# Performance work log

Hardware: AMD Instinct MI355X
Metric: run time of the kernel (lower is better)

Reference implementation:

```python
import jax, jax.numpy as jnp
from jax import lax
import numpy as np

# dims: batch, in_channels, out_channels, spatial, kernel, padding
B, IC, OC, H, W, K, PAD = 4, 64, 64, 32, 32, 3, 1


def setup_inputs() -> dict:
    key = jax.random.key(0)
    k1, k2, k3, k4 = jax.random.split(key, 4)
    # x is a binary (+/-1) activation in this stochastic binary network
    x = jnp.sign(jax.random.normal(k1, (B, IC, H, W), jnp.float32))
    x = jnp.where(x == 0, 1.0, x)
    # q: small per-unit correction probabilities
    q = jax.random.uniform(k2, (B, IC, H, W), jnp.float32) * 1e-3
    # xavier_uniform with sigmoid gain (=1.0), as in _reset_parameters
    fan_in, fan_out = IC * K * K, OC * K * K
    bound = float(np.sqrt(6.0 / (fan_in + fan_out)))
    weight = jax.random.uniform(k3, (OC, IC, K, K), jnp.float32, -bound, bound)
    bbound = float(1.0 / np.sqrt(fan_in))
    bias = jax.random.uniform(k4, (OC,), jnp.float32, -bbound, bbound)
    return {"x": x, "q": q, "weight": weight, "bias": bias}


def _forward(x, q, weight, bias, key):
    pad = 2 * (K // 2) - PAD  # = 1 for k=3, padding=1
    # a0 = conv(x), NCHW / OIHW
    a0 = lax.conv_general_dilated(x, weight, (1, 1), [(PAD, PAD), (PAD, PAD)]) \
         + bias[None, :, None, None]                      # [B,OC,H,W]
    p0 = jax.nn.sigmoid(a0)
    # stochastic binary sample new_x in {-1,+1}; sample is non-differentiable
    new_x = 2.0 * jax.random.bernoulli(key, p0).astype(p0.dtype) - 1.0

    Kf = jnp.flip(weight, (2, 3))                         # flipped kernel
    a0_ = jnp.pad(a0, ((0, 0), (0, 0), (pad, pad), (pad, pad)))     # [B,OC,H+K-1,W+K-1]
    p0_ = jnp.pad(p0, ((0, 0), (0, 0), (pad, pad), (pad, pad)))
    y_ = jnp.pad(new_x, ((0, 0), (0, 0), (pad, pad), (pad, pad)))

    # Fused version of _compute_conv_diffs + _compute_delta_sum: instead of
    # materializing the full [K,K,B,OC,IC,H,W] tensor, process each (l1,l2)
    # shift (K*K = 9 static iterations), same math.
    delta_q = jnp.zeros((B, OC, H + K - 1, W + K - 1), p0.dtype)
    for l1 in range(K):
        for l2 in range(K):
            # a[l1,l2] : pre-activation if input bit (l1,l2) were flipped
            a_l = a0_[:, :, None, l1:l1 + H, l2:l2 + W] \
                  - 2.0 * x[:, None] * Kf[None, :, :, l1, l2, None, None]  # [B,OC,IC,H,W]
            p_l = jax.nn.sigmoid(a_l)
            add = jnp.sum((p_l - p0_[:, :, None, l1:l1 + H, l2:l2 + W]) * q[:, None],
                          axis=2) * (-y_[:, :, l1:l1 + H, l2:l2 + W])       # [B,OC,H,W]
            delta_q = delta_q.at[:, :, l1:l1 + H, l2:l2 + W].add(add)
    delta_q = delta_q[:, :, pad:-pad, pad:-pad]           # [B,OC,H,W]

    # delta_0: zero in value, carries gradient of p0 (straight-through trick)
    delta_0 = -new_x * (p0 - lax.stop_gradient(p0))
    qs = jnp.sum(q, axis=(1, 2, 3), keepdims=True)        # [B,1,1,1]
    new_q = delta_0 * (1.0 - qs) + delta_q
    # stride == 1 -> the [::stride] slicing is a no-op
    return new_x, new_q


def reference(x, q, weight, bias):
    return _forward(x, q, weight, bias, jax.random.key(42))
```

## Files before the change

### kernel.cpp

```cpp
#include <hip/hip_runtime.h>
#include <cstdint>


typedef __attribute__((ext_vector_type(4))) int   i32x4;
typedef __attribute__((ext_vector_type(8))) short s16x8;
typedef __attribute__((ext_vector_type(4))) float f32x4;

static constexpr int OFF_X8   = 0;
static constexpr int OFF_XQH  = 295936;
static constexpr int OFF_WD   = 887808;
static constexpr int OFF_WB   = 1035264;

__device__ __forceinline__ uint32_t rotl32(uint32_t v, int n) {
  return (v << n) | (v >> (32 - n));
}

__device__ __forceinline__ unsigned short f2bf(float f) {
  uint32_t u = __float_as_uint(f);
  uint32_t r = (u + 0x7FFFu + ((u >> 16) & 1u)) >> 16;
  return (unsigned short)r;
}

__device__ __forceinline__ float threefry_u(uint32_t j) {
  uint32_t x0 = 0u, x1 = j;
  const uint32_t ks1 = 42u, ks2 = 0x1BD11BDAu ^ 42u;
  x0 += 0u; x1 += ks1;
#define QR(rot) { x0 += x1; x1 = rotl32(x1, rot); x1 ^= x0; }
  QR(13) QR(15) QR(26) QR(6)
  x0 += ks1; x1 += ks2 + 1u;
  QR(17) QR(29) QR(16) QR(24)
  x0 += ks2; x1 += 0u + 2u;
  QR(13) QR(15) QR(26) QR(6)
  x0 += 0u; x1 += ks1 + 3u;
  QR(17) QR(29) QR(16) QR(24)
  x0 += ks1; x1 += ks2 + 4u;
  QR(13) QR(15) QR(26) QR(6)
  x0 += ks2; x1 += 0u + 5u;
#undef QR
  uint32_t bits = x0 ^ x1;
  return __uint_as_float((bits >> 9) | 0x3F800000u) - 1.0f;
}

__global__ __launch_bounds__(256) void prep_kernel(
    const float* __restrict__ x, const float* __restrict__ q,
    const float* __restrict__ weight, char* __restrict__ ws) {
  const int blk = blockIdx.x;
  const int tid = threadIdx.x;

  if (blk < 128) {
    const int b = blk >> 5;
    const int h = blk & 31;
    __shared__ char           x8s[2048];
    __shared__ unsigned short xqs[2048];
    const int ic = tid >> 2;
    const int w0 = (tid & 3) * 8;
    const int src = ((b * 64 + ic) * 32 + h) * 32 + w0;
    float4 xa = *(const float4*)(x + src);
    float4 xb = *(const float4*)(x + src + 4);
    float4 qa = *(const float4*)(q + src);
    float4 qb = *(const float4*)(q + src + 4);
    float xv[8] = {xa.x, xa.y, xa.z, xa.w, xb.x, xb.y, xb.z, xb.w};
    float qv[8] = {qa.x, qa.y, qa.z, qa.w, qb.x, qb.y, qb.z, qb.w};
#pragma unroll
    for (int j = 0; j < 8; ++j) {
      int a = (w0 + j) * 64 + ic;
      x8s[a] = (char)(int)xv[j];
      xqs[a] = f2bf(xv[j] * qv[j]);
    }
    __syncthreads();
    const int rowel = ((b * 34 + h + 1) * 34 + 1) * 64;
    ((uint2*)(ws + OFF_X8 + rowel))[tid]      = ((const uint2*)x8s)[tid];
    ((uint4*)(ws + OFF_XQH + rowel * 2))[tid] = ((const uint4*)xqs)[tid];
  } else if (blk < 132) {
    const int b = blk - 128;
    for (int k = tid; k < 8448; k += 256) {
      int cell = k >> 6;
      int ic = k & 63;
      int hp, wp;
      if (cell < 34)       { hp = 0;          wp = cell; }
      else if (cell < 68)  { hp = 33;         wp = cell - 34; }
      else if (cell < 100) { hp = cell - 67;  wp = 0; }
      else                 { hp = cell - 99;  wp = 33; }
      int a = ((b * 34 + hp) * 34 + wp) * 64 + ic;
      ((char*)(ws + OFF_X8))[a] = 0;
      ((unsigned short*)(ws + OFF_XQH))[a] = 0;
    }
  } else {
    int k  = (blk - 132) * 256 + tid;
    int ic = k & 63;
    int t  = k >> 6;
    int oc  = t & 63;
    int tap = t >> 6;
    int kh = tap / 3, kw = tap % 3;
    float Wv = weight[((oc * 64 + ic) * 3 + kh) * 3 + kw];
    long long wi = llrint((double)Wv * 2147483648.0);
    char* wd = ws + OFF_WD;
#pragma unroll
    for (int dig = 0; dig < 4; ++dig) {
      signed char d = (signed char)(wi & 0xFF);
      wd[dig * 36864 + k] = d;
      wi = (wi - (long long)d) >> 8;
    }
    ((unsigned short*)(ws + OFF_WB))[k]  = f2bf(Wv);
  }
}

__global__ __launch_bounds__(256, 1) void main_kernel(
    const char* __restrict__ ws, const float* __restrict__ bias,
    float* __restrict__ out) {
  const char* x8            = ws + OFF_X8;
  const unsigned short* xqh = (const unsigned short*)(ws + OFF_XQH);
  const char* wd            = ws + OFF_WD;
  const unsigned short* wb  = (const unsigned short*)(ws + OFF_WB);

  const int b  = blockIdx.x >> 6;
  const int h  = (blockIdx.x >> 1) & 31;
  const int nt = blockIdx.x & 1;

  const int octile = threadIdx.x >> 6;
  const int lane   = threadIdx.x & 63;
  const int quad   = lane >> 4;
  const int l16    = lane & 15;

  i32x4 bI[9];
  s16x8 bX[9][2];
#pragma unroll
  for (int kh = 0; kh < 3; ++kh) {
#pragma unroll
    for (int kw = 0; kw < 3; ++kw) {
      const int t = kh * 3 + kw;
      const int pix = ((b * 34 + h + kh) * 34 + (nt * 16 + l16 + kw)) * 64;
      bI[t]    = *(const i32x4*)(x8 + pix + quad * 16);
      bX[t][0] = *(const s16x8*)(xqh + pix + quad * 8);
      bX[t][1] = *(const s16x8*)(xqh + pix + 32 + quad * 8);
    }
  }

  i32x4 accI[4];
#pragma unroll
  for (int d = 0; d < 4; ++d) accI[d] = (i32x4){0, 0, 0, 0};
  f32x4 aC1 = {0.f, 0.f, 0.f, 0.f};

  const int aoff_i8 = (octile * 16 + l16) * 64 + quad * 16;
  const int aoff_bf = (octile * 16 + l16) * 64 + quad * 8;

#pragma unroll
  for (int tap = 0; tap < 9; ++tap) {
    i32x4 aI[4];
#pragma unroll
    for (int d = 0; d < 4; ++d)
      aI[d] = *(const i32x4*)(wd + d * 36864 + tap * 4096 + aoff_i8);
    s16x8 aW0 = *(const s16x8*)(wb + tap * 4096 + aoff_bf);
    s16x8 aW1 = *(const s16x8*)(wb + tap * 4096 + aoff_bf + 32);
#pragma unroll
    for (int d = 0; d < 4; ++d)
      accI[d] = __builtin_amdgcn_mfma_i32_16x16x64_i8(aI[d], bI[tap], accI[d], 0, 0, 0);
    aC1 = __builtin_amdgcn_mfma_f32_16x16x32_bf16(aW0, bX[tap][0], aC1, 0, 0, 0);
    aC1 = __builtin_amdgcn_mfma_f32_16x16x32_bf16(aW1, bX[tap][1], aC1, 0, 0, 0);
  }

  const int w = nt * 16 + l16;
#pragma unroll
  for (int r = 0; r < 4; ++r) {
    const int ocr = octile * 16 + quad * 4 + r;
    double a0 = (((double)accI[3][r] * 256.0 + (double)accI[2][r]) * 256.0 +
                 (double)accI[1][r]) * 256.0 + (double)accI[0][r];
    a0 = a0 * (1.0 / 2147483648.0) + (double)bias[ocr];
    double p0d = 1.0 / (1.0 + exp(-a0));
    const int o = ((b * 64 + ocr) * 32 + h) * 32 + w;
    float su = threefry_u((uint32_t)o);
    float nx = ((double)su < p0d) ? 1.0f : -1.0f;
    float p0 = (float)p0d;
    float s1 = p0 * (1.0f - p0);
    float dq = 2.0f * nx * s1 * aC1[r];
    out[o] = nx;
    out[262144 + o] = dq;
  }
}

extern "C" void kernel_launch(void* const* d_in, const int* in_sizes, int n_in,
                              void* d_out, int out_size, void* d_ws, size_t ws_size,
                              hipStream_t stream) {
  const float* x      = (const float*)d_in[0];
  const float* q      = (const float*)d_in[1];
  const float* weight = (const float*)d_in[2];
  const float* bias   = (const float*)d_in[3];
  float* out = (float*)d_out;
  char* ws   = (char*)d_ws;

  prep_kernel<<<276, 256, 0, stream>>>(x, q, weight, ws);
  main_kernel<<<256, 256, 0, stream>>>(ws, bias, out);
}
```

Measured before the change: 71.16 us.

## Fuse activation repacking into main kernel via padded shared-memory tiles

```diff
diff --git a/kernel.cpp b/kernel.cpp
--- a/kernel.cpp
+++ b/kernel.cpp
@@ -6,10 +6,11 @@
 typedef __attribute__((ext_vector_type(8))) short s16x8;
 typedef __attribute__((ext_vector_type(4))) float f32x4;
 
-static constexpr int OFF_X8   = 0;
-static constexpr int OFF_XQH  = 295936;
-static constexpr int OFF_WD   = 887808;
-static constexpr int OFF_WB   = 1035264;
+static constexpr int OFF_WD = 0;
+static constexpr int OFF_WB = 147456;
+
+static constexpr int X8_STRIDE = 80;
+static constexpr int XQ_STRIDE = 72;
 
 __device__ __forceinline__ uint32_t rotl32(uint32_t v, int n) {
   return (v << n) | (v >> (32 - n));
@@ -41,87 +42,82 @@
   return __uint_as_float((bits >> 9) | 0x3F800000u) - 1.0f;
 }
 
-__global__ __launch_bounds__(256) void prep_kernel(
-    const float* __restrict__ x, const float* __restrict__ q,
+__global__ __launch_bounds__(256) void wprep_kernel(
     const float* __restrict__ weight, char* __restrict__ ws) {
-  const int blk = blockIdx.x;
-  const int tid = threadIdx.x;
-
-  if (blk < 128) {
-    const int b = blk >> 5;
-    const int h = blk & 31;
-    __shared__ char           x8s[2048];
-    __shared__ unsigned short xqs[2048];
-    const int ic = tid >> 2;
-    const int w0 = (tid & 3) * 8;
-    const int src = ((b * 64 + ic) * 32 + h) * 32 + w0;
-    float4 xa = *(const float4*)(x + src);
-    float4 xb = *(const float4*)(x + src + 4);
-    float4 qa = *(const float4*)(q + src);
-    float4 qb = *(const float4*)(q + src + 4);
-    float xv[8] = {xa.x, xa.y, xa.z, xa.w, xb.x, xb.y, xb.z, xb.w};
-    float qv[8] = {qa.x, qa.y, qa.z, qa.w, qb.x, qb.y, qb.z, qb.w};
+  int k  = blockIdx.x * 256 + threadIdx.x;
+  int ic = k & 63;
+  int t  = k >> 6;
+  int oc  = t & 63;
+  int tap = t >> 6;
+  int kh = tap / 3, kw = tap % 3;
+  float Wv = weight[((oc * 64 + ic) * 3 + kh) * 3 + kw];
+  long long wi = llrint((double)Wv * 2147483648.0);
+  char* wd = ws + OFF_WD;
 #pragma unroll
-    for (int j = 0; j < 8; ++j) {
-      int a = (w0 + j) * 64 + ic;
-      x8s[a] = (char)(int)xv[j];
-      xqs[a] = f2bf(xv[j] * qv[j]);
-    }
-    __syncthreads();
-    const int rowel = ((b * 34 + h + 1) * 34 + 1) * 64;
-    ((uint2*)(ws + OFF_X8 + rowel))[tid]      = ((const uint2*)x8s)[tid];
-    ((uint4*)(ws + OFF_XQH + rowel * 2))[tid] = ((const uint4*)xqs)[tid];
-  } else if (blk < 132) {
-    const int b = blk - 128;
-    for (int k = tid; k < 8448; k += 256) {
-      int cell = k >> 6;
-      int ic = k & 63;
-      int hp, wp;
-      if (cell < 34)       { hp = 0;          wp = cell; }
-      else if (cell < 68)  { hp = 33;         wp = cell - 34; }
-      else if (cell < 100) { hp = cell - 67;  wp = 0; }
-      else                 { hp = cell - 99;  wp = 33; }
-      int a = ((b * 34 + hp) * 34 + wp) * 64 + ic;
-      ((char*)(ws + OFF_X8))[a] = 0;
-      ((unsigned short*)(ws + OFF_XQH))[a] = 0;
-    }
-  } else {
-    int k  = (blk - 132) * 256 + tid;
-    int ic = k & 63;
-    int t  = k >> 6;
-    int oc  = t & 63;
-    int tap = t >> 6;
-    int kh = tap / 3, kw = tap % 3;
-    float Wv = weight[((oc * 64 + ic) * 3 + kh) * 3 + kw];
-    long long wi = llrint((double)Wv * 2147483648.0);
-    char* wd = ws + OFF_WD;
-#pragma unroll
-    for (int dig = 0; dig < 4; ++dig) {
-      signed char d = (signed char)(wi & 0xFF);
-      wd[dig * 36864 + k] = d;
-      wi = (wi - (long long)d) >> 8;
-    }
-    ((unsigned short*)(ws + OFF_WB))[k]  = f2bf(Wv);
+  for (int dig = 0; dig < 4; ++dig) {
+    signed char d = (signed char)(wi & 0xFF);
+    wd[dig * 36864 + k] = d;
+    wi = (wi - (long long)d) >> 8;
   }
+  ((unsigned short*)(ws + OFF_WB))[k] = f2bf(Wv);
 }
 
 __global__ __launch_bounds__(256, 1) void main_kernel(
+    const float* __restrict__ x, const float* __restrict__ q,
     const char* __restrict__ ws, const float* __restrict__ bias,
     float* __restrict__ out) {
-  const char* x8            = ws + OFF_X8;
-  const unsigned short* xqh = (const unsigned short*)(ws + OFF_XQH);
-  const char* wd            = ws + OFF_WD;
-  const unsigned short* wb  = (const unsigned short*)(ws + OFF_WB);
+  const char* wd           = ws + OFF_WD;
+  const unsigned short* wb = (const unsigned short*)(ws + OFF_WB);
+
+  __shared__ __align__(16) char           x8s[3 * 34 * X8_STRIDE];
+  __shared__ __align__(16) unsigned short xqs[3 * 34 * XQ_STRIDE];
 
   const int b  = blockIdx.x >> 6;
   const int h  = (blockIdx.x >> 1) & 31;
   const int nt = blockIdx.x & 1;
+  const int tid = threadIdx.x;
 
-  const int octile = threadIdx.x >> 6;
-  const int lane   = threadIdx.x & 63;
+  {
+    int* z1 = (int*)x8s;
+#pragma unroll
+    for (int i = tid; i < 3 * 34 * X8_STRIDE / 4; i += 256) z1[i] = 0;
+    int* z2 = (int*)xqs;
+#pragma unroll
+    for (int i = tid; i < 3 * 34 * XQ_STRIDE / 2; i += 256) z2[i] = 0;
+  }
+  __syncthreads();
+
+  {
+    const int ic = tid >> 2;
+    const int w0 = (tid & 3) * 8;
+#pragma unroll
+    for (int r = 0; r < 3; ++r) {
+      const int hg = h - 1 + r;
+      if (hg >= 0 && hg < 32) {
+        const int src = ((b * 64 + ic) * 32 + hg) * 32 + w0;
+        float4 xa = *(const float4*)(x + src);
+        float4 xb = *(const float4*)(x + src + 4);
+        float4 qa = *(const float4*)(q + src);
+        float4 qb = *(const float4*)(q + src + 4);
+        float xv[8] = {xa.x, xa.y, xa.z, xa.w, xb.x, xb.y, xb.z, xb.w};
+        float qv[8] = {qa.x, qa.y, qa.z, qa.w, qb.x, qb.y, qb.z, qb.w};
+#pragma unroll
+        for (int j = 0; j < 8; ++j) {
+          const int wp = w0 + j + 1;
+          x8s[(r * 34 + wp) * X8_STRIDE + ic] = (char)(int)xv[j];
+          xqs[(r * 34 + wp) * XQ_STRIDE + ic] = f2bf(xv[j] * qv[j]);
+        }
+      }
+    }
+  }
+  __syncthreads();
+
+  const int octile = tid >> 6;
+  const int lane   = tid & 63;
   const int quad   = lane >> 4;
   const int l16    = lane & 15;
 
+  const int pxbase = nt * 16 + l16;
   i32x4 bI[9];
   s16x8 bX[9][2];
 #pragma unroll
@@ -129,10 +125,10 @@
 #pragma unroll
     for (int kw = 0; kw < 3; ++kw) {
       const int t = kh * 3 + kw;
-      const int pix = ((b * 34 + h + kh) * 34 + (nt * 16 + l16 + kw)) * 64;
-      bI[t]    = *(const i32x4*)(x8 + pix + quad * 16);
-      bX[t][0] = *(const s16x8*)(xqh + pix + quad * 8);
-      bX[t][1] = *(const s16x8*)(xqh + pix + 32 + quad * 8);
+      const int px = kh * 34 + pxbase + kw;
+      bI[t]    = *(const i32x4*)&x8s[px * X8_STRIDE + quad * 16];
+      bX[t][0] = *(const s16x8*)&xqs[px * XQ_STRIDE + quad * 8];
+      bX[t][1] = *(const s16x8*)&xqs[px * XQ_STRIDE + 32 + quad * 8];
     }
   }
 
@@ -188,6 +184,6 @@
   float* out = (float*)d_out;
   char* ws   = (char*)d_ws;
 
-  prep_kernel<<<276, 256, 0, stream>>>(x, q, weight, ws);
-  main_kernel<<<256, 256, 0, stream>>>(ws, bias, out);
+  wprep_kernel<<<144, 256, 0, stream>>>(weight, ws);
+  main_kernel<<<256, 256, 0, stream>>>(x, q, ws, bias, out);
 }
```

Result: no change. 69.97 us (-1.7%).
